# Performance work log

Measured on AMD Instinct MI355X. Metric: run time of the kernel, lower is better.

## Reference

```python
import jax, jax.numpy as jnp
import numpy as np

HEADS = 4
OUT_CH = 32
NEG_SLOPE = 0.2  # PyG GATConv default leaky_relu slope


def setup_inputs() -> dict:
    key = jax.random.key(0)
    ks = jax.random.split(key, 8)
    N, E, C_IN = 500000, 1500000, 128
    x = jax.random.normal(ks[0], (N, C_IN), dtype=jnp.float32)
    edge_index = jax.random.randint(ks[1], (2, E), 0, N, dtype=jnp.int64)
    # GATConv params (lin weight, attention vectors, bias)
    W = jax.random.normal(ks[2], (C_IN, HEADS * OUT_CH), dtype=jnp.float32) * (1.0 / np.sqrt(C_IN))
    att_src = jax.random.normal(ks[3], (HEADS, OUT_CH), dtype=jnp.float32) * 0.1
    att_dst = jax.random.normal(ks[4], (HEADS, OUT_CH), dtype=jnp.float32) * 0.1
    bias = jnp.zeros((HEADS * OUT_CH,), dtype=jnp.float32)
    # fc head
    fc_w = jax.random.normal(ks[5], (HEADS * OUT_CH, 1), dtype=jnp.float32) * (1.0 / np.sqrt(HEADS * OUT_CH))
    fc_b = jnp.zeros((1,), dtype=jnp.float32)
    return {"x": x, "edge_index": edge_index, "W": W, "att_src": att_src,
            "att_dst": att_dst, "bias": bias, "fc_w": fc_w, "fc_b": fc_b}


def reference(x, edge_index, W, att_src, att_dst, bias, fc_w, fc_b):
    N = x.shape[0]
    # PyG GATConv adds self-loops by default
    loops = jnp.arange(N, dtype=edge_index.dtype)
    src = jnp.concatenate([edge_index[0], loops])  # [Etot]
    dst = jnp.concatenate([edge_index[1], loops])  # [Etot]

    h = (x @ W).reshape(N, HEADS, OUT_CH)                # [N,H,C]
    a_src = jnp.einsum('nhc,hc->nh', h, att_src)          # [N,H]
    a_dst = jnp.einsum('nhc,hc->nh', h, att_dst)          # [N,H]

    e = a_src[src] + a_dst[dst]                           # [Etot,H]
    e = jax.nn.leaky_relu(e, NEG_SLOPE)
    # segment softmax over incoming edges of each dst node
    e_max = jax.ops.segment_max(e, dst, num_segments=N)   # [N,H]
    e_exp = jnp.exp(e - e_max[dst])
    e_sum = jax.ops.segment_sum(e_exp, dst, num_segments=N)
    alpha = e_exp / e_sum[dst]                            # [Etot,H]

    msg = h[src] * alpha[:, :, None]                      # [Etot,H,C]
    out = jax.ops.segment_sum(msg, dst, num_segments=N)   # [N,H,C]
    out = out.reshape(N, HEADS * OUT_CH) + bias

    out = jax.nn.relu(out)
    logits = out @ fc_w + fc_b                            # [N,1]
    return jax.nn.sigmoid(logits)
```

## Files before the change

kernel.cpp:

```cpp
#include <hip/hip_runtime.h>

typedef __attribute__((ext_vector_type(8))) short bf16x8;
typedef __attribute__((ext_vector_type(4))) float f32x4;

__device__ __forceinline__ unsigned short f2bf(float f){
  unsigned int u = __builtin_bit_cast(unsigned int, f);
  u += 0x7fffu + ((u >> 16) & 1u);
  return (unsigned short)(u >> 16);
}
__device__ __forceinline__ float bf_lo(unsigned int v){
  return __builtin_bit_cast(float, v << 16);
}
__device__ __forceinline__ float bf_hi(unsigned int v){
  return __builtin_bit_cast(float, v & 0xffff0000u);
}
__device__ __forceinline__ float lrelu(float x){ return x > 0.f ? x : 0.2f * x; }

#define GLOAD_LDS16(g, l) \
  __builtin_amdgcn_global_load_lds((const __attribute__((address_space(1))) unsigned int*)(g), \
                                   (__attribute__((address_space(3))) unsigned int*)(l), 16, 0, 0)

__global__ __launch_bounds__(256) void k_init(const float* __restrict__ W,
                                              unsigned short* __restrict__ WbfT,
                                              int4* __restrict__ deg4, int n4){
  int i = blockIdx.x * 256 + threadIdx.x;
  if (i < n4){ int4 z; z.x=0; z.y=0; z.z=0; z.w=0; deg4[i] = z; }
  if (i < 128*128){
    int c = i & 127, k = i >> 7;
    WbfT[c * 136 + k] = f2bf(W[k * 128 + c]);
  }
}

__global__ __launch_bounds__(256, 2) void k_gemm_hist(
    const float* __restrict__ x, const unsigned short* __restrict__ WbfT,
    const float* __restrict__ attS, const float* __restrict__ attD,
    unsigned short* __restrict__ h, float* __restrict__ aS, float* __restrict__ aD,
    int N, int nslices, int nbGemm,
    const int* __restrict__ dstA, int E, int* __restrict__ deg)
{
  __shared__ float xbuf[4][2][16*128];
  int tid = threadIdx.x;

  if ((int)blockIdx.x >= nbGemm){
    int nb = (int)gridDim.x - nbGemm;
    int bid = (int)blockIdx.x - nbGemm;
    int t0 = bid * 256 + tid;
    int stride = nb * 256;
    int E4 = E >> 2;
    const int4* d4 = (const int4*)dstA;
    for (int i = t0; i < E4; i += stride){
      int4 d = d4[i];
      atomicAdd(&deg[d.x], 1);
      atomicAdd(&deg[d.y], 1);
      atomicAdd(&deg[d.z], 1);
      atomicAdd(&deg[d.w], 1);
    }
    for (int e = (E & ~3) + t0; e < E; e += stride) atomicAdd(&deg[dstA[e]], 1);
    return;
  }

  int wv = tid >> 6, lane = tid & 63;
  int lrow = lane & 15, lgrp = lane >> 4;

  bf16x8 wf[4][8];
  #pragma unroll
  for (int kt = 0; kt < 4; ++kt)
    #pragma unroll
    for (int ct = 0; ct < 8; ++ct)
      wf[kt][ct] = *(const bf16x8*)(WbfT + (ct*16 + lrow) * 136 + kt*32 + lgrp*8);

  int slice  = (int)blockIdx.x * 4 + wv;
  int stride = nbGemm * 4;

  auto STAGE = [&](int s, int b){
    if (s >= nslices) s = nslices - 1;
    char* dst0 = (char*)&xbuf[wv][b][0];
    #pragma unroll
    for (int k = 0; k < 8; ++k){
      int c = k * 64 + lane;
      int r = c >> 5, j = c & 31;
      int gr = s * 16 + r; if (gr >= N) gr = N - 1;
      const char* src = (const char*)(x + (size_t)gr * 128) + ((j ^ (r & 7)) << 4);
      GLOAD_LDS16(src, dst0 + k * 1024);
    }
  };

  STAGE(slice, 0);
  int bi = 0;

  for (int s = slice; s < nslices; s += stride){
    STAGE(s + stride, bi ^ 1);
    asm volatile("s_waitcnt vmcnt(8)" ::: "memory");

    const f32x4* xb = (const f32x4*)&xbuf[wv][bi][0];
    bf16x8 af[4];
    #pragma unroll
    for (int kt = 0; kt < 4; ++kt){
      int j0 = kt * 8 + lgrp * 2;
      f32x4 lo = xb[lrow * 32 + ( j0      ^ (lrow & 7))];
      f32x4 hi = xb[lrow * 32 + ((j0 + 1) ^ (lrow & 7))];
      bf16x8 a;
      #pragma unroll
      for (int j = 0; j < 4; ++j){
        a[j]   = (short)f2bf(lo[j]);
        a[4+j] = (short)f2bf(hi[j]);
      }
      af[kt] = a;
    }

    f32x4 acc[8];
    #pragma unroll
    for (int ct = 0; ct < 8; ++ct){ acc[ct][0]=0.f; acc[ct][1]=0.f; acc[ct][2]=0.f; acc[ct][3]=0.f; }
    #pragma unroll
    for (int kt = 0; kt < 4; ++kt){
      #pragma unroll
      for (int ct = 0; ct < 8; ++ct){
        acc[ct] = __builtin_amdgcn_mfma_f32_16x16x32_bf16(wf[kt][ct], af[kt], acc[ct], 0, 0, 0);
      }
    }

    int row = s * 16 + lrow;
    float ps[4] = {0.f,0.f,0.f,0.f}, pd[4] = {0.f,0.f,0.f,0.f};
    #pragma unroll
    for (int ct = 0; ct < 8; ++ct){
      int hh = ct >> 1;
      f32x4 s4 = *(const f32x4*)(attS + ct*16 + lgrp*4);
      f32x4 d4 = *(const f32x4*)(attD + ct*16 + lgrp*4);
      #pragma unroll
      for (int g = 0; g < 4; ++g){
        ps[hh] += acc[ct][g] * s4[g];
        pd[hh] += acc[ct][g] * d4[g];
      }
    }
    #pragma unroll
    for (int hh = 0; hh < 4; ++hh){
      ps[hh] += __shfl_xor(ps[hh], 16, 64);
      ps[hh] += __shfl_xor(ps[hh], 32, 64);
      pd[hh] += __shfl_xor(pd[hh], 16, 64);
      pd[hh] += __shfl_xor(pd[hh], 32, 64);
    }
    if (lgrp == 0 && row < N){
      f32x4 vs, vd;
      #pragma unroll
      for (int hh = 0; hh < 4; ++hh){ vs[hh] = ps[hh]; vd[hh] = pd[hh]; }
      *(f32x4*)(aS + (size_t)row * 4) = vs;
      *(f32x4*)(aD + (size_t)row * 4) = vd;
    }
    if (row < N){
      unsigned short* hp = h + (size_t)row * 128 + lgrp * 4;
      #pragma unroll
      for (int ct = 0; ct < 8; ++ct){
        unsigned int u0 = (unsigned int)f2bf(acc[ct][0])
                        | ((unsigned int)f2bf(acc[ct][1]) << 16);
        unsigned int u1 = (unsigned int)f2bf(acc[ct][2])
                        | ((unsigned int)f2bf(acc[ct][3]) << 16);
        uint2 u; u.x = u0; u.y = u1;
        *(uint2*)(hp + ct * 16) = u;
      }
    }
    bi ^= 1;
  }
}

__global__ __launch_bounds__(256) void k_chunksum(const int* __restrict__ deg, int N,
                                                  int* __restrict__ bsum){
  __shared__ int sm[256];
  int tid = threadIdx.x;
  int base = blockIdx.x * 2048 + tid * 8;
  int s = 0;
  #pragma unroll
  for (int j = 0; j < 8; ++j) s += (base + j < N) ? deg[base + j] : 0;
  sm[tid] = s; __syncthreads();
  for (int off = 128; off > 0; off >>= 1){
    if (tid < off) sm[tid] += sm[tid + off];
    __syncthreads();
  }
  if (tid == 0) bsum[blockIdx.x] = sm[0];
}

__global__ __launch_bounds__(256) void k_scansums(int* __restrict__ bsum, int nb){
  __shared__ int sm[256];
  int tid = threadIdx.x;
  int carry = 0;
  for (int base = 0; base < nb; base += 256){
    int v = (base + tid < nb) ? bsum[base + tid] : 0;
    sm[tid] = v; __syncthreads();
    for (int off = 1; off < 256; off <<= 1){
      int t = (tid >= off) ? sm[tid - off] : 0;
      __syncthreads();
      sm[tid] += t;
      __syncthreads();
    }
    int incl = sm[tid];
    int total = sm[255];
    __syncthreads();
    if (base + tid < nb) bsum[base + tid] = carry + incl - v;
    carry += total;
  }
}

__global__ __launch_bounds__(256) void k_scanfinal(const int* __restrict__ deg,
    const int* __restrict__ bsum, int N, int E,
    int* __restrict__ rowptr, int* __restrict__ cursor){
  __shared__ int sm[256];
  int tid = threadIdx.x;
  int base = blockIdx.x * 2048 + tid * 8;
  int v[8];
  #pragma unroll
  for (int j = 0; j < 8; ++j) v[j] = (base + j < N) ? deg[base + j] : 0;
  int t = 0;
  #pragma unroll
  for (int j = 0; j < 8; ++j){ int x_ = v[j]; v[j] = t; t += x_; }
  sm[tid] = t; __syncthreads();
  for (int off = 1; off < 256; off <<= 1){
    int u = (tid >= off) ? sm[tid - off] : 0;
    __syncthreads();
    sm[tid] += u;
    __syncthreads();
  }
  int excl = sm[tid] - t;
  int off0 = bsum[blockIdx.x] + excl;
  #pragma unroll
  for (int j = 0; j < 8; ++j){
    if (base + j < N){
      int val = off0 + v[j];
      rowptr[base + j] = val;
      cursor[base + j] = val;
    }
  }
  if (blockIdx.x == 0 && tid == 0) rowptr[N] = E;
}

__global__ __launch_bounds__(256) void k_scatter(const int* __restrict__ src,
    const int* __restrict__ dst, int E, int* __restrict__ cursor,
    const float* __restrict__ aS, const float* __restrict__ aD,
    float* __restrict__ eb){
  int e = blockIdx.x * 256 + threadIdx.x;
  if (e < E){
    int s = src[e], d = dst[e];
    int p = atomicAdd(&cursor[d], 1);
    f32x4 as = *(const f32x4*)(aS + (size_t)s * 4);
    f32x4 ad = *(const f32x4*)(aD + (size_t)d * 4);
    f32x4 w;
    #pragma unroll
    for (int hh = 0; hh < 4; ++hh) w[hh] = __expf(lrelu(as[hh] + ad[hh]));
    float* rec = eb + (size_t)p * 8;
    *(f32x4*)rec = w;
    rec[4] = __builtin_bit_cast(float, s);
  }
}

__global__ __launch_bounds__(256) void k_aggr(
    const uint4* __restrict__ h4, const float* __restrict__ aS,
    const float* __restrict__ aD, const int* __restrict__ rowptr,
    const float* __restrict__ eb, const float* __restrict__ bias,
    const float* __restrict__ fcw, const float* __restrict__ fcb,
    float* __restrict__ out, int N)
{
  int lane = threadIdx.x & 63;
  int l16  = lane & 15;
  int node = ((int)blockIdx.x * 256 + (int)threadIdx.x) >> 4;
  if (node >= N) return;
  int head = l16 >> 2;

  float wself = __expf(lrelu(aS[node * 4 + head] + aD[node * 4 + head]));
  float wsum  = wself;

  float acc[8];
  {
    uint4 hv = h4[node * 16 + l16];
    acc[0] = wself * bf_lo(hv.x);  acc[1] = wself * bf_hi(hv.x);
    acc[2] = wself * bf_lo(hv.y);  acc[3] = wself * bf_hi(hv.y);
    acc[4] = wself * bf_lo(hv.z);  acc[5] = wself * bf_hi(hv.z);
    acc[6] = wself * bf_lo(hv.w);  acc[7] = wself * bf_hi(hv.w);
  }

  int rb = rowptr[node], re = rowptr[node + 1];
  for (int j = rb; j < re; j += 4){
    int i1 = (j + 1 < re) ? j + 1 : j;
    int i2 = (j + 2 < re) ? j + 2 : j;
    int i3 = (j + 3 < re) ? j + 3 : j;
    float m1 = (j + 1 < re) ? 1.f : 0.f;
    float m2 = (j + 2 < re) ? 1.f : 0.f;
    float m3 = (j + 3 < re) ? 1.f : 0.f;
    float w0 = eb[(size_t)j  * 8 + head];
    float w1 = eb[(size_t)i1 * 8 + head] * m1;
    float w2 = eb[(size_t)i2 * 8 + head] * m2;
    float w3 = eb[(size_t)i3 * 8 + head] * m3;
    int s0 = __builtin_bit_cast(int, eb[(size_t)j  * 8 + 4]);
    int s1 = __builtin_bit_cast(int, eb[(size_t)i1 * 8 + 4]);
    int s2 = __builtin_bit_cast(int, eb[(size_t)i2 * 8 + 4]);
    int s3 = __builtin_bit_cast(int, eb[(size_t)i3 * 8 + 4]);
    uint4 v0 = h4[(size_t)s0 * 16 + l16];
    uint4 v1 = h4[(size_t)s1 * 16 + l16];
    uint4 v2 = h4[(size_t)s2 * 16 + l16];
    uint4 v3 = h4[(size_t)s3 * 16 + l16];
    wsum += w0 + w1 + w2 + w3;
    acc[0] += w0*bf_lo(v0.x) + w1*bf_lo(v1.x) + w2*bf_lo(v2.x) + w3*bf_lo(v3.x);
    acc[1] += w0*bf_hi(v0.x) + w1*bf_hi(v1.x) + w2*bf_hi(v2.x) + w3*bf_hi(v3.x);
    acc[2] += w0*bf_lo(v0.y) + w1*bf_lo(v1.y) + w2*bf_lo(v2.y) + w3*bf_lo(v3.y);
    acc[3] += w0*bf_hi(v0.y) + w1*bf_hi(v1.y) + w2*bf_hi(v2.y) + w3*bf_hi(v3.y);
    acc[4] += w0*bf_lo(v0.z) + w1*bf_lo(v1.z) + w2*bf_lo(v2.z) + w3*bf_lo(v3.z);
    acc[5] += w0*bf_hi(v0.z) + w1*bf_hi(v1.z) + w2*bf_hi(v2.z) + w3*bf_hi(v3.z);
    acc[6] += w0*bf_lo(v0.w) + w1*bf_lo(v1.w) + w2*bf_lo(v2.w) + w3*bf_lo(v3.w);
    acc[7] += w0*bf_hi(v0.w) + w1*bf_hi(v1.w) + w2*bf_hi(v2.w) + w3*bf_hi(v3.w);
  }

  float inv = 1.f / wsum;
  const float* bp = bias + l16 * 8;
  const float* fp = fcw  + l16 * 8;
  f32x4 b0 = *(const f32x4*)bp,      b1 = *(const f32x4*)(bp + 4);
  f32x4 f0 = *(const f32x4*)fp,      f1 = *(const f32x4*)(fp + 4);
  float p = 0.f;
  p += fmaxf(acc[0]*inv + b0[0], 0.f) * f0[0];
  p += fmaxf(acc[1]*inv + b0[1], 0.f) * f0[1];
  p += fmaxf(acc[2]*inv + b0[2], 0.f) * f0[2];
  p += fmaxf(acc[3]*inv + b0[3], 0.f) * f0[3];
  p += fmaxf(acc[4]*inv + b1[0], 0.f) * f1[0];
  p += fmaxf(acc[5]*inv + b1[1], 0.f) * f1[1];
  p += fmaxf(acc[6]*inv + b1[2], 0.f) * f1[2];
  p += fmaxf(acc[7]*inv + b1[3], 0.f) * f1[3];
  #pragma unroll
  for (int m = 1; m < 16; m <<= 1) p += __shfl_xor(p, m, 64);
  if (l16 == 0) out[node] = 1.f / (1.f + __expf(-(p + fcb[0])));
}

extern "C" void kernel_launch(void* const* d_in, const int* in_sizes, int n_in,
                              void* d_out, int out_size, void* d_ws, size_t ws_size,
                              hipStream_t stream) {
  const float* x    = (const float*)d_in[0];
  const int*   ei   = (const int*)  d_in[1];
  const float* W    = (const float*)d_in[2];
  const float* attS = (const float*)d_in[3];
  const float* attD = (const float*)d_in[4];
  const float* bias = (const float*)d_in[5];
  const float* fcw  = (const float*)d_in[6];
  const float* fcb  = (const float*)d_in[7];

  int N = in_sizes[0] / 128;
  int E = in_sizes[1] / 2;
  const int* srcA = ei;
  const int* dstA = ei + E;

  char* ws = (char*)d_ws;
  size_t off = 0;
  auto alloc = [&](size_t bytes) -> void* {
    void* p = ws + off;
    off += (bytes + 255) & ~(size_t)255;
    return p;
  };
  unsigned short* h  = (unsigned short*)alloc((size_t)N * 128 * 2);
  float* aS   = (float*)alloc((size_t)N * 4 * 4);
  float* aD   = (float*)alloc((size_t)N * 4 * 4);
  int* deg    = (int*)alloc((size_t)N * 4);
  int* rowptr = (int*)alloc(((size_t)N + 1) * 4);
  int* cursor = (int*)alloc((size_t)N * 4);
  float* eb   = (float*)alloc((size_t)E * 32 + 64);
  int* bsum   = (int*)alloc(4096);
  unsigned short* WbfT = (unsigned short*)alloc(128 * 136 * 2);

  int n4 = (N + 3) / 4;
  int ninit = (n4 > 16384) ? n4 : 16384;
  k_init<<<(ninit + 255) / 256, 256, 0, stream>>>(W, WbfT, (int4*)deg, n4);
  int nslices = (N + 15) / 16;
  int nbGemm = 512, nbHist = 256;
  k_gemm_hist<<<nbGemm + nbHist, 256, 0, stream>>>(x, WbfT, attS, attD, h, aS, aD,
                                                   N, nslices, nbGemm, dstA, E, deg);
  int nb = (N + 2047) / 2048;
  k_chunksum<<<nb, 256, 0, stream>>>(deg, N, bsum);
  k_scansums<<<1, 256, 0, stream>>>(bsum, nb);
  k_scanfinal<<<nb, 256, 0, stream>>>(deg, bsum, N, E, rowptr, cursor);
  k_scatter<<<(E + 255) / 256, 256, 0, stream>>>(srcA, dstA, E, cursor, aS, aD, eb);
  k_aggr<<<(N + 15) / 16, 256, 0, stream>>>((const uint4*)h, aS, aD, rowptr, eb,
                                            bias, fcw, fcb, (float*)d_out, N);
}
```

Measured before the change: 327.9 us.

## Keep W in shared memory and double-buffer x rows in registers

The GEMM part of the fused kernel no longer holds the whole bf16 weight matrix in registers. Each block now copies W once into shared memory and reads the MFMA B fragments from there. The per-wave x staging through LDS via global_load_lds is replaced by direct vector loads into two register buffers, alternating load and compute. Launch bounds are raised to 3 blocks per SM and the GEMM grid grows from 512 to 768 blocks, aiming for more occupancy and latency hiding, at the cost of more LDS reads per MFMA.

```diff
diff --git a/kernel.cpp b/kernel.cpp
--- a/kernel.cpp
+++ b/kernel.cpp
@@ -31,14 +31,14 @@
   }
 }
 
-__global__ __launch_bounds__(256, 2) void k_gemm_hist(
+__global__ __launch_bounds__(256, 3) void k_gemm_hist(
     const float* __restrict__ x, const unsigned short* __restrict__ WbfT,
     const float* __restrict__ attS, const float* __restrict__ attD,
     unsigned short* __restrict__ h, float* __restrict__ aS, float* __restrict__ aD,
     int N, int nslices, int nbGemm,
     const int* __restrict__ dstA, int E, int* __restrict__ deg)
 {
-  __shared__ float xbuf[4][2][16*128];
+  __shared__ unsigned short Wt[128][136];
   int tid = threadIdx.x;
 
   if ((int)blockIdx.x >= nbGemm){
@@ -59,51 +59,41 @@
     return;
   }
 
+  const char* wsrc = (const char*)WbfT;
+  #pragma unroll
+  for (int it = 0; it < 9; ++it){
+    int i = it * 256 + tid;
+    if (i < 2176) GLOAD_LDS16(wsrc + (size_t)i * 16, ((char*)Wt) + i * 16);
+  }
+  __syncthreads();
+
   int wv = tid >> 6, lane = tid & 63;
   int lrow = lane & 15, lgrp = lane >> 4;
 
-  bf16x8 wf[4][8];
-  #pragma unroll
-  for (int kt = 0; kt < 4; ++kt)
-    #pragma unroll
-    for (int ct = 0; ct < 8; ++ct)
-      wf[kt][ct] = *(const bf16x8*)(WbfT + (ct*16 + lrow) * 136 + kt*32 + lgrp*8);
-
   int slice  = (int)blockIdx.x * 4 + wv;
   int stride = nbGemm * 4;
 
-  auto STAGE = [&](int s, int b){
+  auto LOADS = [&](f32x4* v, int s){
     if (s >= nslices) s = nslices - 1;
-    char* dst0 = (char*)&xbuf[wv][b][0];
-    #pragma unroll
-    for (int k = 0; k < 8; ++k){
-      int c = k * 64 + lane;
-      int r = c >> 5, j = c & 31;
-      int gr = s * 16 + r; if (gr >= N) gr = N - 1;
-      const char* src = (const char*)(x + (size_t)gr * 128) + ((j ^ (r & 7)) << 4);
-      GLOAD_LDS16(src, dst0 + k * 1024);
+    int r = s * 16 + lrow; if (r >= N) r = N - 1;
+    const float* xp = x + (size_t)r * 128 + lgrp * 8;
+    #pragma unroll
+    for (int kt = 0; kt < 4; ++kt){
+      v[kt*2]     = *(const f32x4*)(xp + kt * 32);
+      v[kt*2 + 1] = *(const f32x4*)(xp + kt * 32 + 4);
     }
   };
 
-  STAGE(slice, 0);
-  int bi = 0;
-
-  for (int s = slice; s < nslices; s += stride){
-    STAGE(s + stride, bi ^ 1);
-    asm volatile("s_waitcnt vmcnt(8)" ::: "memory");
-
-    const f32x4* xb = (const f32x4*)&xbuf[wv][bi][0];
+  auto COMP = [&](const f32x4* v, int s){
+    if (s >= nslices) return;
     bf16x8 af[4];
     #pragma unroll
     for (int kt = 0; kt < 4; ++kt){
-      int j0 = kt * 8 + lgrp * 2;
-      f32x4 lo = xb[lrow * 32 + ( j0      ^ (lrow & 7))];
-      f32x4 hi = xb[lrow * 32 + ((j0 + 1) ^ (lrow & 7))];
       bf16x8 a;
       #pragma unroll
       for (int j = 0; j < 4; ++j){
-        a[j]   = (short)f2bf(lo[j]);
-        a[4+j] = (short)f2bf(hi[j]);
+        a[j]   = (short)f2bf(v[kt*2][j]);
+        a[4+j] = (short)f2bf(v[kt*2+1][j]);
       }
       af[kt] = a;
     }
@@ -115,7 +105,8 @@
     for (int kt = 0; kt < 4; ++kt){
       #pragma unroll
       for (int ct = 0; ct < 8; ++ct){
-        acc[ct] = __builtin_amdgcn_mfma_f32_16x16x32_bf16(wf[kt][ct], af[kt], acc[ct], 0, 0, 0);
+        bf16x8 bw = *(const bf16x8*)&Wt[ct*16 + lrow][kt*32 + lgrp*8];
+        acc[ct] = __builtin_amdgcn_mfma_f32_16x16x32_bf16(bw, af[kt], acc[ct], 0, 0, 0);
       }
     }
 
@@ -158,7 +149,15 @@
         *(uint2*)(hp + ct * 16) = u;
       }
     }
-    bi ^= 1;
+  };
+
+  f32x4 vA[8], vB[8];
+  LOADS(vA, slice);
+  for (int s = slice; s < nslices; s += 2 * stride){
+    LOADS(vB, s + stride);
+    COMP(vA, s);
+    LOADS(vA, s + 2 * stride);
+    COMP(vB, s + stride);
   }
 }
 
@@ -363,7 +362,7 @@
   int ninit = (n4 > 16384) ? n4 : 16384;
   k_init<<<(ninit + 255) / 256, 256, 0, stream>>>(W, WbfT, (int4*)deg, n4);
   int nslices = (N + 15) / 16;
-  int nbGemm = 512, nbHist = 256;
+  int nbGemm = 768, nbHist = 256;
   k_gemm_hist<<<nbGemm + nbHist, 256, 0, stream>>>(x, WbfT, attS, attD, h, aS, aD,
                                                    N, nslices, nbGemm, dstA, E, deg);
   int nb = (N + 2047) / 2048;
```

After: 449.9 us. 37.2% more time.
